# Optimization experiments

Measured on AMD Instinct MI355X. Metric: run time of the kernel, lower is better.

Reference implementation:

```python
import jax, jax.numpy as jnp
import numpy as np
from jax import lax

L = 2        # encoder layers
D = 256      # d_model
H = 8        # nhead
DH = D // H  # head dim
CF = 2       # compression_factor (default in CustomizedAttn)
FF = 2048    # dim_feedforward
B = 10       # batch (forced: null_k has shape (10,1,D))
HH = 40
WW = 40
T = HH * WW  # seq len = 1600
EPS = 1e-5


def setup_inputs() -> dict:
    key = jax.random.key(0)
    ks = jax.random.split(key, 16)
    f = lambda k, shp: jax.random.normal(k, shp, jnp.float32) * 0.02
    return {
        "src": jax.random.normal(ks[0], (B, D, HH, WW), jnp.float32),
        "pos_embed": jax.random.normal(ks[1], (B, D, HH, WW), jnp.float32),
        "Wq": f(ks[2], (L, D, D)),
        "Wk": f(ks[3], (L, D, D)),
        "Wv": f(ks[4], (L, D, D)),
        "Wo": f(ks[5], (L, D, D)),
        "bo": jnp.zeros((L, D), jnp.float32),
        "conv_w": f(ks[6], (L, D, D // H, CF)),  # grouped Conv1d weight [out, in/groups, k]
        "conv_b": jnp.zeros((L, D), jnp.float32),
        "null_k": f(ks[7], (L, B, 1, D)),
        "null_v": f(ks[8], (L, B, 1, D)),
        "ln1_g": jnp.ones((L, D), jnp.float32),
        "ln1_b": jnp.zeros((L, D), jnp.float32),
        "ln2_g": jnp.ones((L, D), jnp.float32),
        "ln2_b": jnp.zeros((L, D), jnp.float32),
        "W1": f(ks[9], (L, FF, D)),
        "b1": jnp.zeros((L, FF), jnp.float32),
        "W2": f(ks[10], (L, D, FF)),
        "b2": jnp.zeros((L, D), jnp.float32),
    }


def _layernorm(x, g, b):
    m = jnp.mean(x, axis=-1, keepdims=True)
    v = jnp.var(x, axis=-1, keepdims=True)
    return (x - m) * lax.rsqrt(v + EPS) * g + b


def _attn(x, pos, Wq, Wk, Wv, Wo, bo, cw, cb, nk, nv):
    # x, pos: [B, T, D]
    qk = x + pos
    q = qk @ Wq.T
    k = qk @ Wk.T
    v = x @ Wv.T
    # torch: padding = cf - t % cf -> always in [1, cf], so padding ALWAYS applied
    pad = CF - (T % CF)
    k = jnp.pad(k, ((0, 0), (pad, 0), (0, 0)))
    v = jnp.pad(v, ((0, 0), (pad, 0), (0, 0)))

    def compress(t_):  # grouped strided Conv1d over time, shared weights for k and v
        y = lax.conv_general_dilated(
            t_.transpose(0, 2, 1), cw, (CF,), "VALID",
            dimension_numbers=("NCH", "OIH", "NCH"), feature_group_count=H)
        return (y + cb[None, :, None]).transpose(0, 2, 1)

    k = jnp.concatenate([nk, compress(k)], axis=1)  # [B, Tc+10, D]
    v = jnp.concatenate([nv, compress(v)], axis=1)
    split = lambda t_: t_.reshape(B, t_.shape[1], H, DH).transpose(0, 2, 1, 3)
    qh, kh, vh = split(q), split(k), split(v)
    # NOTE: scale uses FULL d_model (d ** -0.5), faithful to the source.
    dots = jnp.einsum("bhid,bhjd->bhij", qh, kh) * (D ** -0.5)
    # NOTE: the source computes softmax(dots) but then overwrites it with
    # dropout(dots); at inference attention weights are the raw scaled dots.
    out = jnp.einsum("bhij,bhjd->bhid", dots, vh)
    out = out.transpose(0, 2, 1, 3).reshape(B, T, D)
    return out @ Wo.T + bo


def reference(src, pos_embed, Wq, Wk, Wv, Wo, bo, conv_w, conv_b, null_k, null_v,
              ln1_g, ln1_b, ln2_g, ln2_b, W1, b1, W2, b2):
    x = src.reshape(B, D, T).transpose(0, 2, 1)        # [B, T, D]
    pos = pos_embed.reshape(B, D, T).transpose(0, 2, 1)
    for l in range(L):
        a = _attn(x, pos, Wq[l], Wk[l], Wv[l], Wo[l], bo[l],
                  conv_w[l], conv_b[l], null_k[l], null_v[l])
        x = _layernorm(x + a, ln1_g[l], ln1_b[l])
        ff = jnp.maximum(x @ W1[l].T + b1[l], 0.0) @ W2[l].T + b2[l]
        x = _layernorm(x + ff, ln2_g[l], ln2_b[l])
    return x.transpose(0, 2, 1).reshape(B, D, HH, WW)
```

## Files before the change

### kernel.cpp

```cpp
#include <hip/hip_runtime.h>
#include <math.h>

typedef __attribute__((ext_vector_type(8))) short short8;
typedef __attribute__((ext_vector_type(4))) short short4v;
typedef __attribute__((ext_vector_type(4))) float f32x4;
typedef unsigned int u32;

constexpr int Bsz = 10;
constexpr int Dm  = 256;
constexpr int Hh  = 8;
constexpr int Tt  = 1600;
constexpr int FFd = 2048;
constexpr int Tkv = 802;
constexpr int JCH = 8;
constexpr size_t Fsz  = (size_t)Bsz * Tt * Dm;
constexpr size_t PAD  = 65536;
constexpr size_t KVsz = (size_t)Bsz * Tkv * Dm;
constexpr size_t FHsz = (size_t)Bsz * Tt * FFd;
constexpr size_t WBsz = 2621440;

__device__ float g_x[Fsz];
__device__ float g_qk[Fsz];
__device__ float g_t[Fsz];
__device__ float g_kc[KVsz];
__device__ float g_vc[KVsz];
__device__ float g_kvm[(size_t)Bsz * Hh * 32 * 32];
__device__ float g_kvp[(size_t)JCH * Bsz * Hh * 32 * 32];
__device__ float g_pos[Fsz];
__device__ unsigned short g_xb[Fsz + PAD];
__device__ unsigned short g_qkb[Fsz + PAD];
__device__ unsigned short g_tb[Fsz + PAD];
__device__ unsigned short g_qb[Fsz + PAD];
__device__ unsigned short g_ffh[FHsz + PAD];
__device__ unsigned short g_wb[WBsz];
__device__ unsigned short g_wo2[(size_t)Bsz * Dm * Dm];

__device__ __forceinline__ float* selbuf(int id) {
  switch (id) {
    case 0: return g_x;
    case 1: return g_qk;
    case 2: return g_t;
    case 3: return g_kc;
    case 4: return g_vc;
    default: return g_kvm;
  }
}
__device__ __forceinline__ unsigned short* selbufb(int id) {
  switch (id) {
    case 0: return g_xb;
    case 1: return g_qkb;
    case 2: return g_tb;
    case 3: return g_ffh;
    default: return g_qb;
  }
}

__device__ __forceinline__ unsigned short f2b(float x) {
  unsigned int u = __float_as_uint(x);
  u += 0x7FFFu + ((u >> 16) & 1u);
  return (unsigned short)(u >> 16);
}
__device__ __forceinline__ float b2f(unsigned short u) {
  return __uint_as_float(((unsigned int)u) << 16);
}

__global__ __launch_bounds__(256) void wconv_all_k(
    const float* __restrict__ Wk, const float* __restrict__ Wq,
    const float* __restrict__ Wv, const float* __restrict__ Wo,
    const float* __restrict__ W1, const float* __restrict__ W2) {
  const int i = blockIdx.x * 256 + threadIdx.x;
  float v;
  if (i < 262144) {
    const int l = i >> 17, r = i & 131071;
    v = (r < 65536) ? Wk[l * 65536 + r] : Wq[l * 65536 + (r - 65536)];
  } else if (i < 393216) {
    v = Wv[i - 262144];
  } else if (i < 524288) {
    v = Wo[i - 393216];
  } else if (i < 1572864) {
    v = W1[i - 524288];
  } else {
    v = W2[i - 1572864];
  }
  g_wb[i] = f2b(v);
}

__global__ __launch_bounds__(256) void trans_in2_k(const float* __restrict__ src,
                                                   const float* __restrict__ pose) {
  __shared__ float ts[32][33];
  __shared__ float tp[32][33];
  const int tx = threadIdx.x & 31, ty = threadIdx.x >> 5;
  const int t0 = blockIdx.x * 32, d0 = blockIdx.y * 32, b = blockIdx.z;
  #pragma unroll
  for (int i = ty; i < 32; i += 8) {
    const size_t gi = ((size_t)(b * Dm + d0 + i)) * Tt + t0 + tx;
    ts[i][tx] = src[gi];
    tp[i][tx] = pose[gi];
  }
  __syncthreads();
  #pragma unroll
  for (int i = ty; i < 32; i += 8) {
    const size_t idx = ((size_t)(b * Tt + t0 + i)) * Dm + d0 + tx;
    const float s = ts[tx][i], p = tp[tx][i];
    g_x[idx] = s;
    g_pos[idx] = p;
    g_xb[idx] = f2b(s);
    g_qkb[idx] = f2b(s + p);
  }
}

__global__ __launch_bounds__(256) void trans_out_k(float* out) {
  __shared__ float tile[32][33];
  const int tx = threadIdx.x & 31, ty = threadIdx.x >> 5;
  const int t0 = blockIdx.x * 32, d0 = blockIdx.y * 32, b = blockIdx.z;
  #pragma unroll
  for (int i = ty; i < 32; i += 8)
    tile[i][tx] = g_x[((size_t)(b * Tt + t0 + i)) * Dm + d0 + tx];
  __syncthreads();
  #pragma unroll
  for (int i = ty; i < 32; i += 8)
    out[((size_t)(b * Dm + d0 + i)) * Tt + t0 + tx] = tile[tx][i];
}

template<int BN, bool DUAL, bool PERB, bool RELU, bool BIAS, bool CBF16>
__global__ __launch_bounds__(256) void gemm2_k(
    int Aid, int woff, const float* __restrict__ bias, int Cid, int C2id,
    int NB, int M, int N, int K) {
  constexpr int BM = 128, BK = 64;
  constexpr int ACH = BM * 8;
  constexpr int BCH = BN * 8;
  constexpr int NW = BN / 32;
  __shared__ short8 As8[2][ACH];
  __shared__ short8 Bs8[2][BCH];
  const int tid = threadIdx.x;
  const int lane = tid & 63, wid = tid >> 6;
  const int wr = wid >> 1, wc = wid & 1;

  const int nwg = gridDim.x;
  const int bid = blockIdx.x;
  const int q = nwg >> 3, r = nwg & 7;
  const int xcd = bid & 7, seq = bid >> 3;
  const int wgid = (xcd < r ? xcd * (q + 1) : r * (q + 1) + (xcd - r) * q) + seq;

  int m0, n0, mlim;
  const unsigned short* W16;
  if constexpr (PERB) {
    const int per = 13 * NB;
    const int b = wgid / per;
    const int rem = wgid - b * per;
    m0 = b * Tt + (rem / NB) * BM;
    n0 = (rem % NB) * BN;
    mlim = b * Tt + Tt;
    W16 = g_wo2 + (size_t)b * 65536;
  } else {
    m0 = (wgid / NB) * BM;
    n0 = (wgid % NB) * BN;
    mlim = M;
    W16 = g_wb + woff;
  }

  const unsigned short* A16 = selbufb(Aid);
  const bool second = DUAL && (n0 >= 256);
  float* Cf = selbuf(second ? C2id : Cid);
  unsigned short* C16 = selbufb(second ? C2id : Cid);
  const int gn0 = second ? n0 - 256 : n0;
  const int cstride = DUAL ? 256 : N;

  f32x4 acc[4][NW];
  #pragma unroll
  for (int m = 0; m < 4; ++m)
    #pragma unroll
    for (int n = 0; n < NW; ++n) acc[m][n] = (f32x4){0.f, 0.f, 0.f, 0.f};

  const int lkc = lane >> 4, lrc = lane & 15;

  auto stage = [&](int t, int buf) {
    const int k0 = t * BK;
    #pragma unroll
    for (int i = 0; i < ACH / 256; ++i) {
      const int c = tid + i * 256;
      const int row = c >> 3, kc = c & 7;
      const unsigned short* gs = A16 + (size_t)(m0 + row) * K + k0 +
                                 ((kc ^ (row & 7)) << 3);
      __builtin_amdgcn_global_load_lds(
          (const __attribute__((address_space(1))) u32*)gs,
          (__attribute__((address_space(3))) u32*)&As8[buf][c], 16, 0, 0);
    }
    #pragma unroll
    for (int i = 0; i < BCH / 256; ++i) {
      const int c = tid + i * 256;
      const int row = c >> 3, kc = c & 7;
      const unsigned short* gs = W16 + (size_t)(n0 + row) * K + k0 +
                                 ((kc ^ (row & 7)) << 3);
      __builtin_amdgcn_global_load_lds(
          (const __attribute__((address_space(1))) u32*)gs,
          (__attribute__((address_space(3))) u32*)&Bs8[buf][c], 16, 0, 0);
    }
  };

  const int nt = K / BK;
  stage(0, 0);
  if (nt > 1) stage(1, 1);
  for (int t = 0; t < nt; ++t) {
    const int cur = t & 1;
    if (t + 1 < nt) {
      if constexpr (BN == 64)
        asm volatile("s_waitcnt vmcnt(6)" ::: "memory");
      else
        asm volatile("s_waitcnt vmcnt(8)" ::: "memory");
    } else {
      asm volatile("s_waitcnt vmcnt(0)" ::: "memory");
    }
    __builtin_amdgcn_sched_barrier(0);
    __builtin_amdgcn_s_barrier();
    #pragma unroll
    for (int kk = 0; kk < 2; ++kk) {
      short8 af[4], bf[NW];
      #pragma unroll
      for (int m = 0; m < 4; ++m) {
        const int r2 = wr * 64 + m * 16 + lrc;
        af[m] = As8[cur][r2 * 8 + ((kk * 4 + lkc) ^ (r2 & 7))];
      }
      #pragma unroll
      for (int n = 0; n < NW; ++n) {
        const int cn = wc * (BN / 2) + n * 16 + lrc;
        bf[n] = Bs8[cur][cn * 8 + ((kk * 4 + lkc) ^ (cn & 7))];
      }
      #pragma unroll
      for (int m = 0; m < 4; ++m)
        #pragma unroll
        for (int n = 0; n < NW; ++n)
          acc[m][n] = __builtin_amdgcn_mfma_f32_16x16x32_bf16(
              af[m], bf[n], acc[m][n], 0, 0, 0);
    }
    __builtin_amdgcn_sched_barrier(0);
    __builtin_amdgcn_s_barrier();
    __builtin_amdgcn_sched_barrier(0);
    if (t + 2 < nt) stage(t + 2, cur);
  }

  constexpr int CSTR = (BN == 64) ? BN + 4 : BN;
  float* ldsC = (float*)&As8[0][0];
  {
    asm volatile("s_waitcnt vmcnt(0)" ::: "memory");
    __builtin_amdgcn_s_barrier();
    const int r0 = lkc * 4;
    #pragma unroll
    for (int m = 0; m < 4; ++m)
      #pragma unroll
      for (int n = 0; n < NW; ++n) {
        const int col = wc * (BN / 2) + n * 16 + lrc;
        #pragma unroll
        for (int j = 0; j < 4; ++j)
          ldsC[(wr * 64 + m * 16 + r0 + j) * CSTR + col] = acc[m][n][j];
      }
    __syncthreads();
  }
  if constexpr (CBF16) {
    constexpr int CH = BM * BN / 8;
    #pragma unroll
    for (int i = 0; i < CH / 256; ++i) {
      const int c = tid + i * 256;
      const int rowl = c / (BN / 8), col8 = (c % (BN / 8)) * 8;
      if (PERB && m0 + rowl >= mlim) continue;
      short8 v;
      #pragma unroll
      for (int j = 0; j < 8; ++j) {
        float x = ldsC[rowl * CSTR + col8 + j];
        if (BIAS) x += bias[gn0 + col8 + j];
        if (RELU) x = fmaxf(x, 0.f);
        v[j] = (short)f2b(x);
      }
      *(short8*)(C16 + (size_t)(m0 + rowl) * cstride + gn0 + col8) = v;
    }
  } else {
    constexpr int CH = BM * BN / 4;
    #pragma unroll
    for (int i = 0; i < CH / 256; ++i) {
      const int c = tid + i * 256;
      const int rowl = c / (BN / 4), col4 = (c % (BN / 4)) * 4;
      if (PERB && m0 + rowl >= mlim) continue;
      float4 v;
      float* pv = &v.x;
      #pragma unroll
      for (int j = 0; j < 4; ++j) {
        float x = ldsC[rowl * CSTR + col4 + j];
        if (BIAS) x += bias[gn0 + col4 + j];
        if (RELU) x = fmaxf(x, 0.f);
        pv[j] = x;
      }
      *(float4*)(Cf + (size_t)(m0 + rowl) * cstride + gn0 + col4) = v;
    }
  }
}

__global__ __launch_bounds__(512, 2) void gemmn_k(
    int Aid, int woff, const float* __restrict__ bias, int K) {
  constexpr int BM = 128, BN = 256, BK = 64;
  constexpr int ACH = BM * 8;
  constexpr int BCH = BN * 8;
  __shared__ short8 As8[2][ACH];
  __shared__ short8 Bs8[2][BCH];
  const int tid = threadIdx.x;
  const int lane = tid & 63, wid = tid >> 6;
  const int wr = wid >> 2, wc = wid & 3;
  const int nwg = gridDim.x, bid = blockIdx.x;
  const int q = nwg >> 3, r = nwg & 7;
  const int xcd = bid & 7, seq = bid >> 3;
  const int wgid = (xcd < r ? xcd * (q + 1) : r * (q + 1) + (xcd - r) * q) + seq;
  const int half = nwg >> 1;
  const int ks = (wgid >= half) ? 1 : 0;
  const int m0 = (wgid - ks * half) * BM;
  const int kbase = ks * (K >> 1);
  const unsigned short* A16 = selbufb(Aid);
  const unsigned short* W16 = g_wb + woff;
  float* Cf = ks ? g_t : g_qk;

  f32x4 acc[4][4];
  #pragma unroll
  for (int m = 0; m < 4; ++m)
    #pragma unroll
    for (int n = 0; n < 4; ++n) acc[m][n] = (f32x4){0.f, 0.f, 0.f, 0.f};

  const int lkc = lane >> 4, lrc = lane & 15;

  auto stage = [&](int t, int buf) {
    const int k0 = kbase + t * BK;
    #pragma unroll
    for (int i = 0; i < ACH / 512; ++i) {
      const int c = tid + i * 512;
      const int row = c >> 3, kc = c & 7;
      const unsigned short* gs = A16 + (size_t)(m0 + row) * K + k0 +
                                 ((kc ^ (row & 7)) << 3);
      __builtin_amdgcn_global_load_lds(
          (const __attribute__((address_space(1))) u32*)gs,
          (__attribute__((address_space(3))) u32*)&As8[buf][c], 16, 0, 0);
    }
    #pragma unroll
    for (int i = 0; i < BCH / 512; ++i) {
      const int c = tid + i * 512;
      const int row = c >> 3, kc = c & 7;
      const unsigned short* gs = W16 + (size_t)row * K + k0 +
                                 ((kc ^ (row & 7)) << 3);
      __builtin_amdgcn_global_load_lds(
          (const __attribute__((address_space(1))) u32*)gs,
          (__attribute__((address_space(3))) u32*)&Bs8[buf][c], 16, 0, 0);
    }
  };

  const int nt = (K >> 1) / BK;
  stage(0, 0);
  stage(1, 1);
  for (int t = 0; t < nt; ++t) {
    const int cur = t & 1;
    if (t + 1 < nt) asm volatile("s_waitcnt vmcnt(6)" ::: "memory");
    else            asm volatile("s_waitcnt vmcnt(0)" ::: "memory");
    __builtin_amdgcn_sched_barrier(0);
    __builtin_amdgcn_s_barrier();
    #pragma unroll
    for (int kk = 0; kk < 2; ++kk) {
      short8 af[4], bf[4];
      #pragma unroll
      for (int m = 0; m < 4; ++m) {
        const int r2 = wr * 64 + m * 16 + lrc;
        af[m] = As8[cur][r2 * 8 + ((kk * 4 + lkc) ^ (r2 & 7))];
      }
      #pragma unroll
      for (int n = 0; n < 4; ++n) {
        const int cn = wc * 64 + n * 16 + lrc;
        bf[n] = Bs8[cur][cn * 8 + ((kk * 4 + lkc) ^ (cn & 7))];
      }
      #pragma unroll
      for (int m = 0; m < 4; ++m)
        #pragma unroll
        for (int n = 0; n < 4; ++n)
          acc[m][n] = __builtin_amdgcn_mfma_f32_16x16x32_bf16(
              af[m], bf[n], acc[m][n], 0, 0, 0);
    }
    __builtin_amdgcn_sched_barrier(0);
    __builtin_amdgcn_s_barrier();
    __builtin_amdgcn_sched_barrier(0);
    if (t + 2 < nt) stage(t + 2, cur);
  }

  const int r0 = lkc * 4;
  #pragma unroll
  for (int m = 0; m < 4; ++m) {
    const int gm = m0 + wr * 64 + m * 16 + r0;
    #pragma unroll
    for (int n = 0; n < 4; ++n) {
      const int gn = wc * 64 + n * 16 + lrc;
      const float bb = (ks == 0) ? bias[gn] : 0.f;
      #pragma unroll
      for (int j = 0; j < 4; ++j)
        Cf[(size_t)(gm + j) * BN + gn] = acc[m][n][j] + bb;
    }
  }
}

template<bool RELU, bool BIAS, bool CBF16>
__global__ __launch_bounds__(512, 4) void gemmh_k(
    int Aid, int woff, const float* __restrict__ bias, int Cid,
    int NB, int M, int N) {
  constexpr int BM = 128, BN = 128, K = 256, KH = 128;
  __shared__ short8 As8[BM * 16];
  __shared__ short8 Bs8[BN * 16];
  const int tid = threadIdx.x;
  const int lane = tid & 63, wid = tid >> 6;
  const int wr = wid >> 2, wc = wid & 3;
  const int nwg = gridDim.x;
  const int bid = blockIdx.x;
  const int q = nwg >> 3, r = nwg & 7;
  const int xcd = bid & 7, seq = bid >> 3;
  const int wgid = (xcd < r ? xcd * (q + 1) : r * (q + 1) + (xcd - r) * q) + seq;
  const int m0 = (wgid / NB) * BM, n0 = (wgid % NB) * BN;
  const unsigned short* A16 = selbufb(Aid);
  const unsigned short* W16 = g_wb + woff;
  float* Cf = selbuf(Cid);
  unsigned short* C16 = selbufb(Cid);
  const int lkc = lane >> 4, lrc = lane & 15;

  f32x4 acc[4][2];
  #pragma unroll
  for (int m = 0; m < 4; ++m)
    #pragma unroll
    for (int n = 0; n < 2; ++n) acc[m][n] = (f32x4){0.f, 0.f, 0.f, 0.f};

  #pragma unroll
  for (int h = 0; h < 2; ++h) {
    const int k0 = h * KH;
    if (h) __builtin_amdgcn_s_barrier();
    #pragma unroll
    for (int i = 0; i < (BM * 16) / 512; ++i) {
      const int c = tid + i * 512;
      const int row = c >> 4, kc = c & 15;
      const unsigned short* gs = A16 + (size_t)(m0 + row) * K + k0 +
                                 ((kc ^ (row & 15)) << 3);
      __builtin_amdgcn_global_load_lds(
          (const __attribute__((address_space(1))) u32*)gs,
          (__attribute__((address_space(3))) u32*)&As8[c], 16, 0, 0);
    }
    #pragma unroll
    for (int i = 0; i < (BN * 16) / 512; ++i) {
      const int c = tid + i * 512;
      const int row = c >> 4, kc = c & 15;
      const unsigned short* gs = W16 + (size_t)(n0 + row) * K + k0 +
                                 ((kc ^ (row & 15)) << 3);
      __builtin_amdgcn_global_load_lds(
          (const __attribute__((address_space(1))) u32*)gs,
          (__attribute__((address_space(3))) u32*)&Bs8[c], 16, 0, 0);
    }
    asm volatile("s_waitcnt vmcnt(0)" ::: "memory");
    __builtin_amdgcn_sched_barrier(0);
    __builtin_amdgcn_s_barrier();

    __builtin_amdgcn_s_setprio(1);
    #pragma unroll
    for (int s = 0; s < 4; ++s) {
      short8 af[4], bf[2];
      #pragma unroll
      for (int m = 0; m < 4; ++m) {
        const int r2 = wr * 64 + m * 16 + lrc;
        af[m] = As8[r2 * 16 + ((s * 4 + lkc) ^ (r2 & 15))];
      }
      #pragma unroll
      for (int n = 0; n < 2; ++n) {
        const int cn = wc * 32 + n * 16 + lrc;
        bf[n] = Bs8[cn * 16 + ((s * 4 + lkc) ^ (cn & 15))];
      }
      #pragma unroll
      for (int m = 0; m < 4; ++m)
        #pragma unroll
        for (int n = 0; n < 2; ++n)
          acc[m][n] = __builtin_amdgcn_mfma_f32_16x16x32_bf16(
              af[m], bf[n], acc[m][n], 0, 0, 0);
    }
    __builtin_amdgcn_s_setprio(0);
  }

  const int r0 = lkc * 4;
  #pragma unroll
  for (int m = 0; m < 4; ++m) {
    const int gmb = m0 + wr * 64 + m * 16 + r0;
    #pragma unroll
    for (int n = 0; n < 2; ++n) {
      const int gn = n0 + wc * 32 + n * 16 + lrc;
      const float bb = BIAS ? bias[gn] : 0.f;
      #pragma unroll
      for (int j = 0; j < 4; ++j) {
        float v = acc[m][n][j] + bb;
        if (RELU) v = fmaxf(v, 0.f);
        if (CBF16) C16[(size_t)(gmb + j) * N + gn] = f2b(v);
        else       Cf[(size_t)(gmb + j) * N + gn] = v;
      }
    }
  }
}

__global__ __launch_bounds__(256) void compress2_k(
    const float* __restrict__ cw, const float* __restrict__ cb,
    const float* __restrict__ nk, const float* __restrict__ nv) {
  __shared__ float rows[32][256];
  const int tc0 = 1 + blockIdx.x * 16;
  const int b = blockIdx.y;
  const int z = blockIdx.z;
  const int tid = threadIdx.x;
  const int o = tid;
  const int g = o >> 5;

  const unsigned short* srcbuf = z ? g_ffh : g_tb;
  const float* nul = z ? nv : nk;
  float* outb = (z ? g_vc : g_kc) + (size_t)b * Tkv * Dm;

  const int r0g = 2 * tc0 - 2;
  const unsigned short* src = srcbuf + ((size_t)b * Tt + r0g) * Dm;
  #pragma unroll
  for (int i = 0; i < 4; ++i) {
    const int c = tid + i * 256;
    const int row = c >> 5, off = (c & 31) * 8;
    short8 v = *(const short8*)(src + (size_t)row * 256 + off);
    #pragma unroll
    for (int j = 0; j < 8; ++j)
      rows[row][off + j] = b2f((unsigned short)v[j]);
  }

  float we[32], wo[32];
  {
    const float4* wp = (const float4*)(cw + o * 64);
    #pragma unroll
    for (int i = 0; i < 16; ++i) {
      float4 w4 = wp[i];
      we[i * 2 + 0] = w4.x; wo[i * 2 + 0] = w4.y;
      we[i * 2 + 1] = w4.z; wo[i * 2 + 1] = w4.w;
    }
  }
  const float bias = cb[o];
  if (blockIdx.x == 0) {
    outb[o] = nul[b * Dm + o];
    outb[Dm + o] = bias;
  }
  __syncthreads();

  float* outp = outb + o;
  #pragma unroll
  for (int t = 0; t < 16; ++t) {
    const int lr = 2 * t;
    const float* p0 = &rows[lr][g * 32];
    const float* p1 = &rows[lr + 1][g * 32];
    float acc = bias;
    #pragma unroll
    for (int i4 = 0; i4 < 8; ++i4) {
      float4 a0 = *(const float4*)(p0 + i4 * 4);
      float4 a1 = *(const float4*)(p1 + i4 * 4);
      acc = fmaf(we[i4 * 4 + 0], a0.x, acc);
      acc = fmaf(we[i4 * 4 + 1], a0.y, acc);
      acc = fmaf(we[i4 * 4 + 2], a0.z, acc);
      acc = fmaf(we[i4 * 4 + 3], a0.w, acc);
      acc = fmaf(wo[i4 * 4 + 0], a1.x, acc);
      acc = fmaf(wo[i4 * 4 + 1], a1.y, acc);
      acc = fmaf(wo[i4 * 4 + 2], a1.z, acc);
      acc = fmaf(wo[i4 * 4 + 3], a1.w, acc);
    }
    outp[(size_t)(1 + tc0 + t) * Dm] = acc;
  }
}

__global__ __launch_bounds__(256) void kvout1_k() {
  __shared__ float kl[8][32];
  __shared__ float vl[8][32];
  const int bh = blockIdx.x;
  const int js = blockIdx.y;
  const int b = bh >> 3, h = bh & 7;
  const int j0 = js * 101;
  const int jend = (j0 + 101 < Tkv) ? j0 + 101 : Tkv;

  const int tid = threadIdx.x;
  const int lr = tid >> 5;
  const int lc = tid & 31;
  const int e = tid >> 3;
  const int d0 = (tid & 7) * 4;

  float a0 = 0.f, a1 = 0.f, a2 = 0.f, a3 = 0.f;
  const size_t base = (size_t)b * Tkv * Dm + h * 32;

  for (int jc = j0; jc < jend; jc += 8) {
    const int jr = jc + lr;
    if (jr < jend) {
      kl[lr][lc] = g_kc[base + (size_t)jr * Dm + lc];
      vl[lr][lc] = g_vc[base + (size_t)jr * Dm + lc];
    } else {
      kl[lr][lc] = 0.f;
      vl[lr][lc] = 0.f;
    }
    __syncthreads();
    #pragma unroll
    for (int r = 0; r < 8; ++r) {
      const float kf = kl[r][e];
      const float* vr = &vl[r][d0];
      a0 = fmaf(kf, vr[0], a0);
      a1 = fmaf(kf, vr[1], a1);
      a2 = fmaf(kf, vr[2], a2);
      a3 = fmaf(kf, vr[3], a3);
    }
    __syncthreads();
  }
  float* op = g_kvp + ((size_t)js * 80 + bh) * 1024 + e * 32 + d0;
  op[0] = a0; op[1] = a1; op[2] = a2; op[3] = a3;
}

__global__ __launch_bounds__(256) void kvout2_k() {
  const int bh = blockIdx.x;
  const int tid = threadIdx.x;
  const int e = tid >> 3;
  const int d0 = (tid & 7) * 4;
  float a0 = 0.f, a1 = 0.f, a2 = 0.f, a3 = 0.f;
  #pragma unroll
  for (int s = 0; s < JCH; ++s) {
    const float* p = g_kvp + ((size_t)s * 80 + bh) * 1024 + e * 32 + d0;
    a0 += p[0]; a1 += p[1]; a2 += p[2]; a3 += p[3];
  }
  float* op = g_kvm + (size_t)bh * 1024 + e * 32 + d0;
  op[0] = a0 * 0.0625f;
  op[1] = a1 * 0.0625f;
  op[2] = a2 * 0.0625f;
  op[3] = a3 * 0.0625f;
}

__global__ __launch_bounds__(256) void wo2_k(int wooff) {
  const int n = blockIdx.x, b = blockIdx.y;
  const int he = threadIdx.x;
  const int h = he >> 5, e = he & 31;
  const float* kp = g_kvm + ((size_t)(b * Hh + h) * 32 + e) * 32;
  const unsigned short* wp = g_wb + wooff + (size_t)n * Dm + h * 32;
  float acc = 0.f;
  #pragma unroll
  for (int d = 0; d < 32; ++d) acc = fmaf(kp[d], b2f(wp[d]), acc);
  g_wo2[(size_t)b * 65536 + (size_t)n * Dm + he] = f2b(acc);
}

__global__ __launch_bounds__(256) void ln_k(int did, int did2, const float* g,
                                            const float* beta, int do_pos) {
  const int lane = threadIdx.x & 63;
  const int wave = threadIdx.x >> 6;
  const size_t row = (size_t)blockIdx.x * 4 + wave;
  float4 xv = ((const float4*)g_x)[row * 64 + lane];
  float4 dv = ((const float4*)selbuf(did))[row * 64 + lane];
  float v[4] = {xv.x + dv.x, xv.y + dv.y, xv.z + dv.z, xv.w + dv.w};
  if (did2 >= 0) {
    float4 d2 = ((const float4*)selbuf(did2))[row * 64 + lane];
    v[0] += d2.x; v[1] += d2.y; v[2] += d2.z; v[3] += d2.w;
  }
  float sum = v[0] + v[1] + v[2] + v[3];
  float sq = v[0]*v[0] + v[1]*v[1] + v[2]*v[2] + v[3]*v[3];
  #pragma unroll
  for (int off = 32; off; off >>= 1) {
    sum += __shfl_xor(sum, off);
    sq  += __shfl_xor(sq, off);
  }
  const float mean = sum * (1.f / 256.f);
  const float var = sq * (1.f / 256.f) - mean * mean;
  const float rs = rsqrtf(var + 1e-5f);
  float4 gg = ((const float4*)g)[lane];
  float4 bb = ((const float4*)beta)[lane];
  float4 ov;
  ov.x = (v[0] - mean) * rs * gg.x + bb.x;
  ov.y = (v[1] - mean) * rs * gg.y + bb.y;
  ov.z = (v[2] - mean) * rs * gg.z + bb.z;
  ov.w = (v[3] - mean) * rs * gg.w + bb.w;
  ((float4*)g_x)[row * 64 + lane] = ov;
  short4v sv;
  sv[0] = (short)f2b(ov.x); sv[1] = (short)f2b(ov.y);
  sv[2] = (short)f2b(ov.z); sv[3] = (short)f2b(ov.w);
  *(short4v*)&g_xb[(row * 64 + lane) * 4] = sv;
  if (do_pos) {
    float4 pv = ((const float4*)g_pos)[row * 64 + lane];
    short4v qv;
    qv[0] = (short)f2b(ov.x + pv.x); qv[1] = (short)f2b(ov.y + pv.y);
    qv[2] = (short)f2b(ov.z + pv.z); qv[3] = (short)f2b(ov.w + pv.w);
    *(short4v*)&g_qkb[(row * 64 + lane) * 4] = qv;
  }
}

extern "C" void kernel_launch(void* const* d_in, const int* in_sizes, int n_in,
                              void* d_out, int out_size, void* d_ws, size_t ws_size,
                              hipStream_t stream) {
  const float* src  = (const float*)d_in[0];
  const float* pose = (const float*)d_in[1];
  const float* Wq   = (const float*)d_in[2];
  const float* Wk   = (const float*)d_in[3];
  const float* Wv   = (const float*)d_in[4];
  const float* Wo   = (const float*)d_in[5];
  const float* bo   = (const float*)d_in[6];
  const float* cw   = (const float*)d_in[7];
  const float* cb   = (const float*)d_in[8];
  const float* nk   = (const float*)d_in[9];
  const float* nv   = (const float*)d_in[10];
  const float* ln1g = (const float*)d_in[11];
  const float* ln1b = (const float*)d_in[12];
  const float* ln2g = (const float*)d_in[13];
  const float* ln2b = (const float*)d_in[14];
  const float* W1   = (const float*)d_in[15];
  const float* b1   = (const float*)d_in[16];
  const float* W2   = (const float*)d_in[17];
  const float* b2   = (const float*)d_in[18];

  const int MT = Bsz * Tt;
  const dim3 tgrid(Tt / 32, Dm / 32, Bsz);

  const int OV = 262144, OO = 393216, O1 = 524288, O2 = 1572864;
  wconv_all_k<<<10240, 256, 0, stream>>>(Wk, Wq, Wv, Wo, W1, W2);
  trans_in2_k<<<tgrid, 256, 0, stream>>>(src, pose);

  const int MB = MT / 128;
  for (int l = 0; l < 2; ++l) {
    const float* bo_l = bo + (size_t)l * Dm;
    const float* cw_l = cw + (size_t)l * Dm * 64;
    const float* cb_l = cb + (size_t)l * Dm;
    const float* nk_l = nk + (size_t)l * Bsz * Dm;
    const float* nv_l = nv + (size_t)l * Bsz * Dm;
    const float* b1_l = b1 + (size_t)l * FFd;
    const float* b2_l = b2 + (size_t)l * Dm;
    const int wkq = l * 131072;
    const int wv = OV + l * 65536, wo = OO + l * 65536;
    const int w1 = O1 + l * 524288, w2 = O2 + l * 524288;

    gemm2_k<64, true, false, false, false, true><<<8 * MB, 256, 0, stream>>>(
        1, wkq, nullptr, 2, 4, 8, MT, 512, Dm);
    gemm2_k<64, false, false, false, false, true><<<4 * MB, 256, 0, stream>>>(
        0, wv, nullptr, 3, 3, 4, MT, Dm, Dm);
    compress2_k<<<dim3(50, Bsz, 2), 256, 0, stream>>>(cw_l, cb_l, nk_l, nv_l);
    kvout1_k<<<dim3(Bsz * Hh, JCH), 256, 0, stream>>>();
    kvout2_k<<<Bsz * Hh, 256, 0, stream>>>();
    wo2_k<<<dim3(Dm, Bsz), 256, 0, stream>>>(wo);
    gemm2_k<64, false, true, false, true, false><<<Bsz * 13 * 4, 256, 0, stream>>>(
        4, 0, bo_l, 2, 2, 4, MT, Dm, Dm);
    ln_k<<<MT / 4, 256, 0, stream>>>(2, -1, ln1g + l * Dm, ln1b + l * Dm, 0);

    gemmh_k<true, true, true><<<16 * MB, 512, 0, stream>>>(
        0, w1, b1_l, 3, 16, MT, FFd);
    gemmn_k<<<2 * MB, 512, 0, stream>>>(3, w2, b2_l, FFd);
    ln_k<<<MT / 4, 256, 0, stream>>>(1, 2, ln2g + l * Dm, ln2b + l * Dm,
                                     l == 0 ? 1 : 0);
  }

  trans_out_k<<<tgrid, 256, 0, stream>>>((float*)d_out);
}
```

Baseline: 385.2 us.

## Triple-buffer gemm2 LDS pipeline and retile FFN down-projection to 128x128 blocks

gemm2_k moves from a double-buffered LDS pipeline to a triple-buffered one. The next stage load is now issued right after the barrier, before the MFMA work, so one barrier per K-step is removed and loads overlap compute further ahead. The W2 split-K GEMM is retiled from 128x256 blocks of 512 threads to 128x128 blocks of 256 threads, doubling the grid to improve occupancy and load balance. gemmh_k is renamed and its unused M parameter dropped. The extra LDS buffer raises shared memory use per block, which may lower occupancy for gemm2. The vmcnt wait for BN=128 instances of gemm2 changes from 8 to 6, which may be wrong for that tile size.

```diff
diff --git a/kernel.cpp b/kernel.cpp
--- a/kernel.cpp
+++ b/kernel.cpp
@@ -130,8 +130,8 @@
   constexpr int ACH = BM * 8;
   constexpr int BCH = BN * 8;
   constexpr int NW = BN / 32;
-  __shared__ short8 As8[2][ACH];
-  __shared__ short8 Bs8[2][BCH];
+  __shared__ short8 As8[3][ACH];
+  __shared__ short8 Bs8[3][BCH];
   const int tid = threadIdx.x;
   const int lane = tid & 63, wid = tid >> 6;
   const int wr = wid >> 1, wc = wid & 1;
@@ -201,18 +201,17 @@
   const int nt = K / BK;
   stage(0, 0);
   if (nt > 1) stage(1, 1);
+  int cur = 0, nxt = 2;
   for (int t = 0; t < nt; ++t) {
-    const int cur = t & 1;
     if (t + 1 < nt) {
-      if constexpr (BN == 64)
-        asm volatile("s_waitcnt vmcnt(6)" ::: "memory");
-      else
-        asm volatile("s_waitcnt vmcnt(8)" ::: "memory");
+      asm volatile("s_waitcnt vmcnt(6)" ::: "memory");
     } else {
       asm volatile("s_waitcnt vmcnt(0)" ::: "memory");
     }
     __builtin_amdgcn_sched_barrier(0);
     __builtin_amdgcn_s_barrier();
+    __builtin_amdgcn_sched_barrier(0);
+    if (t + 2 < nt) stage(t + 2, nxt);
     #pragma unroll
     for (int kk = 0; kk < 2; ++kk) {
       short8 af[4], bf[NW];
@@ -233,10 +232,8 @@
           acc[m][n] = __builtin_amdgcn_mfma_f32_16x16x32_bf16(
               af[m], bf[n], acc[m][n], 0, 0, 0);
     }
-    __builtin_amdgcn_sched_barrier(0);
-    __builtin_amdgcn_s_barrier();
-    __builtin_amdgcn_sched_barrier(0);
-    if (t + 2 < nt) stage(t + 2, cur);
+    cur = (cur == 2) ? 0 : cur + 1;
+    nxt = (nxt == 2) ? 0 : nxt + 1;
   }
 
   constexpr int CSTR = (BN == 64) ? BN + 4 : BN;
@@ -294,23 +291,25 @@
   }
 }
 
-__global__ __launch_bounds__(512, 2) void gemmn_k(
+__global__ __launch_bounds__(256) void gemmw_k(
     int Aid, int woff, const float* __restrict__ bias, int K) {
-  constexpr int BM = 128, BN = 256, BK = 64;
+  constexpr int BM = 128, BN = 128, BK = 64, NB = 2;
   constexpr int ACH = BM * 8;
   constexpr int BCH = BN * 8;
   __shared__ short8 As8[2][ACH];
   __shared__ short8 Bs8[2][BCH];
   const int tid = threadIdx.x;
   const int lane = tid & 63, wid = tid >> 6;
-  const int wr = wid >> 2, wc = wid & 3;
+  const int wr = wid >> 1, wc = wid & 1;
   const int nwg = gridDim.x, bid = blockIdx.x;
   const int q = nwg >> 3, r = nwg & 7;
   const int xcd = bid & 7, seq = bid >> 3;
   const int wgid = (xcd < r ? xcd * (q + 1) : r * (q + 1) + (xcd - r) * q) + seq;
   const int half = nwg >> 1;
   const int ks = (wgid >= half) ? 1 : 0;
-  const int m0 = (wgid - ks * half) * BM;
+  const int rem = wgid - ks * half;
+  const int m0 = (rem / NB) * BM;
+  const int n0 = (rem % NB) * BN;
   const int kbase = ks * (K >> 1);
   const unsigned short* A16 = selbufb(Aid);
   const unsigned short* W16 = g_wb + woff;
@@ -327,8 +326,8 @@
   auto stage = [&](int t, int buf) {
     const int k0 = kbase + t * BK;
     #pragma unroll
-    for (int i = 0; i < ACH / 512; ++i) {
-      const int c = tid + i * 512;
+    for (int i = 0; i < ACH / 256; ++i) {
+      const int c = tid + i * 256;
       const int row = c >> 3, kc = c & 7;
       const unsigned short* gs = A16 + (size_t)(m0 + row) * K + k0 +
                                  ((kc ^ (row & 7)) << 3);
@@ -337,10 +336,10 @@
           (__attribute__((address_space(3))) u32*)&As8[buf][c], 16, 0, 0);
     }
     #pragma unroll
-    for (int i = 0; i < BCH / 512; ++i) {
-      const int c = tid + i * 512;
+    for (int i = 0; i < BCH / 256; ++i) {
+      const int c = tid + i * 256;
       const int row = c >> 3, kc = c & 7;
-      const unsigned short* gs = W16 + (size_t)row * K + k0 +
+      const unsigned short* gs = W16 + (size_t)(n0 + row) * K + k0 +
                                  ((kc ^ (row & 7)) << 3);
       __builtin_amdgcn_global_load_lds(
           (const __attribute__((address_space(1))) u32*)gs,
@@ -353,7 +352,7 @@
   stage(1, 1);
   for (int t = 0; t < nt; ++t) {
     const int cur = t & 1;
-    if (t + 1 < nt) asm volatile("s_waitcnt vmcnt(6)" ::: "memory");
+    if (t + 1 < nt) asm volatile("s_waitcnt vmcnt(8)" ::: "memory");
     else            asm volatile("s_waitcnt vmcnt(0)" ::: "memory");
     __builtin_amdgcn_sched_barrier(0);
     __builtin_amdgcn_s_barrier();
@@ -389,19 +388,19 @@
     const int gm = m0 + wr * 64 + m * 16 + r0;
     #pragma unroll
     for (int n = 0; n < 4; ++n) {
-      const int gn = wc * 64 + n * 16 + lrc;
+      const int gn = n0 + wc * 64 + n * 16 + lrc;
       const float bb = (ks == 0) ? bias[gn] : 0.f;
       #pragma unroll
       for (int j = 0; j < 4; ++j)
-        Cf[(size_t)(gm + j) * BN + gn] = acc[m][n][j] + bb;
+        Cf[(size_t)(gm + j) * 256 + gn] = acc[m][n][j] + bb;
     }
   }
 }
 
 template<bool RELU, bool BIAS, bool CBF16>
-__global__ __launch_bounds__(512, 4) void gemmh_k(
+__global__ __launch_bounds__(512, 4) void gemmr_k(
     int Aid, int woff, const float* __restrict__ bias, int Cid,
-    int NB, int M, int N) {
+    int NB, int N) {
   constexpr int BM = 128, BN = 128, K = 256, KH = 128;
   __shared__ short8 As8[BM * 16];
   __shared__ short8 Bs8[BN * 16];
@@ -736,9 +735,9 @@
         4, 0, bo_l, 2, 2, 4, MT, Dm, Dm);
     ln_k<<<MT / 4, 256, 0, stream>>>(2, -1, ln1g + l * Dm, ln1b + l * Dm, 0);
 
-    gemmh_k<true, true, true><<<16 * MB, 512, 0, stream>>>(
-        0, w1, b1_l, 3, 16, MT, FFd);
-    gemmn_k<<<2 * MB, 512, 0, stream>>>(3, w2, b2_l, FFd);
+    gemmr_k<true, true, true><<<16 * MB, 512, 0, stream>>>(
+        0, w1, b1_l, 3, 16, FFd);
+    gemmw_k<<<4 * MB, 256, 0, stream>>>(3, w2, b2_l, FFd);
     ln_k<<<MT / 4, 256, 0, stream>>>(1, 2, ln2g + l * Dm, ln2b + l * Dm,
                                      l == 0 ? 1 : 0);
   }
```

After: 376.4 us. -2.3%, faster.
